# Optimization experiments

Measured on AMD Instinct MI355X. Metric: run time of the kernel, lower is better.

Reference implementation:

```python
import jax, jax.numpy as jnp
import numpy as np


def setup_inputs() -> dict:
    key = jax.random.key(0)
    ks = jax.random.split(key, 8)
    B, L, D = 4, 2048, 2048
    H, Dh, S = 24, 64, 64
    Di = H * Dh              # 1536
    P = H * (1 + 2 * S)      # 3096
    return {
        "hidden_states": jax.random.normal(ks[0], (B, L, D), jnp.float32),
        "norm_w": jnp.ones((D,), jnp.float32),
        "in_proj_w": jax.random.normal(ks[1], (2 * Di, D), jnp.float32) * 0.02,
        "in_proj_b": jnp.zeros((2 * Di,), jnp.float32),
        "conv_w": jax.random.normal(ks[2], (Di, 1, 4), jnp.float32) * 0.2,
        "conv_b": jnp.zeros((Di,), jnp.float32),
        "x_proj_w": jax.random.normal(ks[3], (P, Di), jnp.float32) * 0.02,
        "x_proj_b": jnp.zeros((P,), jnp.float32),
        "A_log": jnp.full((H,), np.log(0.5), jnp.float32),
        "log2_alpha_base": jnp.full((H,), -1.0, jnp.float32),
        "log2_beta": jnp.zeros((H,), jnp.float32),
        "surprise_ema": jnp.ones((H,), jnp.float32),
        "out_proj_w": jax.random.normal(ks[4], (D, Di), jnp.float32) * 0.02,
        "out_proj_b": jnp.zeros((D,), jnp.float32),
        "res_gate": jnp.full((1,), 1.0 / np.sqrt(2 * 24), jnp.float32),
    }


def reference(hidden_states, norm_w, in_proj_w, in_proj_b, conv_w, conv_b,
              x_proj_w, x_proj_b, A_log, log2_alpha_base, log2_beta,
              surprise_ema, out_proj_w, out_proj_b, res_gate):
    Bsz, L, D = hidden_states.shape
    H = A_log.shape[0]
    S = (x_proj_b.shape[0] // H - 1) // 2
    Di = in_proj_w.shape[0] // 2
    Dh = Di // H
    eps = jnp.finfo(jnp.float32).eps

    # RMSNorm
    x = hidden_states * jax.lax.rsqrt(jnp.mean(hidden_states ** 2, -1, keepdims=True) + eps) * norm_w
    # in_proj -> split x/z
    xz = x @ in_proj_w.T + in_proj_b
    x, z = xz[..., :Di], xz[..., Di:]
    # causal depthwise conv1d (kernel 4, left pad 3 == torch pad=3 then [:, :L])
    xc = jax.lax.conv_general_dilated(
        x.transpose(0, 2, 1), conv_w, (1,), [(3, 0)],
        dimension_numbers=("NCH", "OIH", "NCH"), feature_group_count=Di)
    x = jax.nn.silu((xc + conv_b[None, :, None]).transpose(0, 2, 1))
    # x_proj -> dt, B, C
    xp = (x @ x_proj_w.T + x_proj_b).reshape(Bsz, L, H, 1 + 2 * S)
    dt = xp[..., 0]
    Bs = xp[..., 1:1 + S]
    Cs = xp[..., 1 + S:]
    Bs = Bs / jnp.maximum(jnp.linalg.norm(Bs, axis=-1, keepdims=True), 1e-12)
    Cs = Cs / jnp.maximum(jnp.linalg.norm(Cs, axis=-1, keepdims=True), 1e-12)
    # dt-scaled log decay (dt_scale = softplus(dt))
    A = jnp.clip(A_log, -2.3, -0.01)[None, None, :] * jax.nn.softplus(dt)
    A_decay = jnp.exp(A)                       # [B, L, H]
    X = x.reshape(Bsz, L, H, Dh)

    # surprise-gate constants (eval mode: EMA buffer fixed)
    alpha_base = 1.0 - 2.0 ** jnp.clip(log2_alpha_base, -3.32, -0.015)   # [H]
    beta = 2.0 ** jnp.clip(log2_beta, -2.0, 2.0)                          # [H]

    def step(carry, xs):
        h, h_red = carry                      # [B,H,S,Dh], [B,H,S]
        x_t, a_t, B_t, C_t = xs               # [B,H,Dh], [B,H], [B,H,S], [B,H,S]
        u_red = B_t * x_t.mean(-1)[..., None]                 # mean over Dh of outer product
        diff = (1.0 - a_t)[..., None] * u_red                 # h_new_reduced - h_expected
        pe = jnp.mean(diff ** 2, -1)                          # [B,H]
        ns = pe / (surprise_ema[None, :] + 1e-6)
        boost = jax.nn.relu(jnp.tanh(beta[None, :] * ns))
        alpha = jnp.clip(alpha_base[None, :] + (1.0 - alpha_base[None, :]) * boost, 0.01, 0.999)
        u_t = B_t[..., None] * x_t[:, :, None, :]             # [B,H,S,Dh]
        h = alpha[..., None, None] * h + (1.0 - alpha)[..., None, None] * u_t
        h_red = h.mean(-1)
        y = jnp.einsum("bhs,bhsd->bhd", C_t, h)
        return (h, h_red), y

    h0 = jnp.zeros((Bsz, H, S, Dh), jnp.float32)
    hr0 = jnp.zeros((Bsz, H, S), jnp.float32)
    xs = (X.transpose(1, 0, 2, 3), A_decay.transpose(1, 0, 2),
          Bs.transpose(1, 0, 2, 3), Cs.transpose(1, 0, 2, 3))
    _, Yt = jax.lax.scan(step, (h0, hr0), xs)                 # [L,B,H,Dh]
    Y = Yt.transpose(1, 0, 2, 3).reshape(Bsz, L, Di)
    Y = Y * jax.nn.silu(z)
    out = Y @ out_proj_w.T + out_proj_b
    return hidden_states + res_gate * out
```

## Files before the change

kernel.cpp:

```cpp
#include <hip/hip_runtime.h>
#include <stdint.h>

#define BB 4
#define LLEN 2048
#define DMODEL 2048
#define NH 24
#define DH 64
#define SS 64
#define DI 1536
#define N2 3072
#define NP 3096
#define NP_PAD 3200
#define MROWS 8192
#define NCHUNK 16
#define QC 128
#define XP2LD 136
#define WBLK 56064

using bf16x8 = __bf16 __attribute__((ext_vector_type(8)));
using f32x4  = float __attribute__((ext_vector_type(4)));

__device__ __forceinline__ unsigned short f2bf(float f) {
  union { float f; unsigned int u; } v; v.f = f;
  unsigned int u = v.u + 0x7fffu + ((v.u >> 16) & 1u);
  return (unsigned short)(u >> 16);
}
__device__ __forceinline__ float bf2f(unsigned short h) {
  union { unsigned int u; float f; } v; v.u = ((unsigned int)h) << 16;
  return v.f;
}

__device__ __forceinline__ void gload16(const void* g, void* l) {
  __builtin_amdgcn_global_load_lds(
    reinterpret_cast<const __attribute__((address_space(1))) void*>(reinterpret_cast<uintptr_t>(g)),
    reinterpret_cast<__attribute__((address_space(3))) void*>((uint32_t)(reinterpret_cast<uintptr_t>(l))),
    16, 0, 0);
}

__global__ __launch_bounds__(256) void k_pre(
    const float* __restrict__ in_w, unsigned short* __restrict__ wA,
    const float* __restrict__ xw, unsigned short* __restrict__ wX,
    const float* __restrict__ ow, unsigned short* __restrict__ wO,
    const float* __restrict__ hs, const float* __restrict__ norm_w,
    unsigned short* __restrict__ xnorm,
    const float* __restrict__ A_log, const float* __restrict__ l2ab,
    const float* __restrict__ l2b, const float* __restrict__ se,
    float* __restrict__ hc) {
  const int blk = blockIdx.x;
  const int t = threadIdx.x;
  if (blk < WBLK) {
    int i = blk * 256 + t;
    if (i < N2 * DMODEL) { wA[i] = f2bf(in_w[i]); return; }
    i -= N2 * DMODEL;
    if (i < NP_PAD * DI) { wX[i] = (i < NP * DI) ? f2bf(xw[i]) : (unsigned short)0; return; }
    i -= NP_PAD * DI;
    wO[i] = f2bf(ow[i]);
    return;
  }
  if (blk == WBLK + MROWS) {
    if (t < NH) {
      hc[t]          = fminf(fmaxf(A_log[t], -2.3f), -0.01f);
      hc[NH + t]     = exp2f(fminf(fmaxf(l2b[t], -2.f), 2.f));
      hc[2 * NH + t] = 1.f - exp2f(fminf(fmaxf(l2ab[t], -3.32f), -0.015f));
      hc[3 * NH + t] = 1.f / (se[t] + 1e-6f);
    }
    return;
  }
  const int row = blk - WBLK;
  const float* x = hs + (size_t)row * DMODEL;
  float4 v0 = reinterpret_cast<const float4*>(x)[t * 2 + 0];
  float4 v1 = reinterpret_cast<const float4*>(x)[t * 2 + 1];
  float ss = v0.x * v0.x + v0.y * v0.y + v0.z * v0.z + v0.w * v0.w +
             v1.x * v1.x + v1.y * v1.y + v1.z * v1.z + v1.w * v1.w;
#pragma unroll
  for (int o = 32; o; o >>= 1) ss += __shfl_xor(ss, o);
  __shared__ float red[4];
  if ((t & 63) == 0) red[t >> 6] = ss;
  __syncthreads();
  ss = red[0] + red[1] + red[2] + red[3];
  const float r = rsqrtf(ss * (1.0f / DMODEL) + 1.1920928955078125e-07f);
  float4 w0 = reinterpret_cast<const float4*>(norm_w)[t * 2 + 0];
  float4 w1 = reinterpret_cast<const float4*>(norm_w)[t * 2 + 1];
  union { unsigned short u[8]; uint4 v; } pk;
  pk.u[0] = f2bf(v0.x * r * w0.x); pk.u[1] = f2bf(v0.y * r * w0.y);
  pk.u[2] = f2bf(v0.z * r * w0.z); pk.u[3] = f2bf(v0.w * r * w0.w);
  pk.u[4] = f2bf(v1.x * r * w1.x); pk.u[5] = f2bf(v1.y * r * w1.y);
  pk.u[6] = f2bf(v1.z * r * w1.z); pk.u[7] = f2bf(v1.w * r * w1.w);
  *reinterpret_cast<uint4*>(xnorm + (size_t)row * DMODEL + t * 8) = pk.v;
}

template <int EPI>
__global__ __launch_bounds__(512, 2)
void k_gemm6(const unsigned short* __restrict__ A, const unsigned short* __restrict__ B,
             const float* __restrict__ bias, void* __restrict__ Cv,
             const float* __restrict__ resid, const float* __restrict__ gatep,
             float* __restrict__ dtbuf,
             int K, int NT_N, int Nout, int ldc) {
  constexpr int AELEM = 128 * 64;
  constexpr int BUFE = AELEM + 16384;
  __shared__ alignas(16) unsigned short sm[3 * BUFE];
  const int tid = threadIdx.x;
  const int lane = tid & 63, wid = tid >> 6;
  const int wm = wid >> 2, wn = wid & 3;
  const int fr = lane & 15, kg = lane >> 4;
  const int nwg = gridDim.x;
  const int wg = ((int)blockIdx.x & 7) * (nwg >> 3) + ((int)blockIdx.x >> 3);
  const int m0 = (wg / NT_N) * 128, n0 = (wg % NT_N) * 256;
  const int NT = K >> 6;

  const unsigned short* asrc[2];
  const unsigned short* bsrc[4];
#pragma unroll
  for (int li = 0; li < 2; ++li) {
    const int gi = li * 512 + tid, r = gi >> 3, q = gi & 7;
    asrc[li] = A + (size_t)(m0 + r) * K + ((q ^ (r & 7)) << 3);
  }
#pragma unroll
  for (int li = 0; li < 4; ++li) {
    const int gi = li * 512 + tid, r = gi >> 3, q = gi & 7;
    bsrc[li] = B + (size_t)(n0 + r) * K + ((q ^ (r & 7)) << 3);
  }
  const int wlds = wid * 64;

#define STG6(buf, ko)                                                          \
  { unsigned short* da_ = sm + (buf) * BUFE;                                   \
    gload16(asrc[0] + (ko), da_ + ((0 * 512 + wlds) << 3));                    \
    gload16(asrc[1] + (ko), da_ + ((1 * 512 + wlds) << 3));                    \
    unsigned short* db_ = sm + (buf) * BUFE + AELEM;                           \
    _Pragma("unroll") for (int li = 0; li < 4; ++li)                           \
      gload16(bsrc[li] + (ko), db_ + ((li * 512 + wlds) << 3)); }

#define ARD6(bufp, f, kk)                                                      \
  (*(const bf16x8*)((bufp) + (wm * 64 + (f) * 16 + fr) * 64 +                  \
      ((((kk) * 4 + kg) ^ (fr & 7)) << 3)))
#define BRD6(bufp, nf, kk)                                                     \
  (*(const bf16x8*)((bufp) + AELEM + (wn * 64 + (nf) * 16 + fr) * 64 +         \
      ((((kk) * 4 + kg) ^ (fr & 7)) << 3)))

  f32x4 acc[4][4] = {};

  STG6(0, 0)
  STG6(1, 64)
  asm volatile("s_waitcnt vmcnt(6)" ::: "memory");
  __builtin_amdgcn_s_barrier();

  int bc_i = 0;
  for (int t = 0; t < NT; ++t) {
    unsigned short* bc = sm + bc_i * BUFE;
    const int bn_i = (bc_i + 2 >= 3) ? (bc_i - 1) : (bc_i + 2);
    const bool st = (t + 2) < NT;
    if (st) STG6(bn_i, (t + 2) << 6)

    bf16x8 bfv[4][2], af[4][2];
#pragma unroll
    for (int nf = 0; nf < 4; ++nf) {
      bfv[nf][0] = BRD6(bc, nf, 0);
      bfv[nf][1] = BRD6(bc, nf, 1);
    }
#pragma unroll
    for (int mf = 0; mf < 4; ++mf) {
      af[mf][0] = ARD6(bc, mf, 0);
      af[mf][1] = ARD6(bc, mf, 1);
    }
    __builtin_amdgcn_sched_barrier(0);
    asm volatile("s_waitcnt lgkmcnt(0)" ::: "memory");
    __builtin_amdgcn_sched_barrier(0);
    __builtin_amdgcn_s_setprio(1);
#pragma unroll
    for (int mf = 0; mf < 4; ++mf)
#pragma unroll
      for (int nf = 0; nf < 4; ++nf)
#pragma unroll
        for (int kk = 0; kk < 2; ++kk)
          acc[mf][nf] = __builtin_amdgcn_mfma_f32_16x16x32_bf16(
              af[mf][kk], bfv[nf][kk], acc[mf][nf], 0, 0, 0);
    __builtin_amdgcn_s_setprio(0);

    if (st) { asm volatile("s_waitcnt vmcnt(6)" ::: "memory"); }
    else    { asm volatile("s_waitcnt vmcnt(0)" ::: "memory"); }
    __builtin_amdgcn_s_barrier();
    bc_i = (bc_i + 1 >= 3) ? 0 : (bc_i + 1);
  }

  float* Cf = (float*)Cv;
  unsigned short* Ch = (unsigned short*)Cv;
  const float rg = (EPI == 2) ? gatep[0] : 0.f;
#pragma unroll
  for (int nf = 0; nf < 4; ++nf) {
    const int col = n0 + wn * 64 + nf * 16 + fr;
    if (col >= Nout) continue;
    const float bv = bias[col];
    if (EPI == 3) {
      const int h = col / 129;
      const int e = col - h * 129;
      if (e == 0) {
#pragma unroll
        for (int mf = 0; mf < 4; ++mf) {
          const int rowb = m0 + wm * 64 + mf * 16 + kg * 4;
#pragma unroll
          for (int r = 0; r < 4; ++r) {
            const int row = rowb + r;
            const size_t r2 = (((size_t)((row >> 11) * NH + h)) << 11) + (row & (LLEN - 1));
            dtbuf[r2] = acc[mf][nf][r] + bv;
          }
        }
      } else {
        const int ep = e - 1;
#pragma unroll
        for (int mf = 0; mf < 4; ++mf) {
          const int rowb = m0 + wm * 64 + mf * 16 + kg * 4;
#pragma unroll
          for (int r = 0; r < 4; ++r) {
            const int row = rowb + r;
            const size_t dst =
                (((size_t)((row >> 11) * NH + h) << 11) + (row & (LLEN - 1))) * XP2LD + ep;
            Ch[dst] = f2bf(acc[mf][nf][r] + bv);
          }
        }
      }
    } else {
#pragma unroll
      for (int mf = 0; mf < 4; ++mf) {
        const int rowb = m0 + wm * 64 + mf * 16 + kg * 4;
#pragma unroll
        for (int r = 0; r < 4; ++r) {
          const size_t o = (size_t)(rowb + r) * ldc + col;
          float v = acc[mf][nf][r] + bv;
          if (EPI == 1) {
            Ch[o] = f2bf(v);
          } else {
            v = resid[o] + rg * v;
            Cf[o] = v;
          }
        }
      }
    }
  }
#undef STG6
#undef ARD6
#undef BRD6
}

__global__ __launch_bounds__(256) void k_alpha(const float* __restrict__ dtbuf,
                                               const float* __restrict__ xmean,
                                               const float* __restrict__ hc,
                                               float* __restrict__ al) {
  const int i = blockIdx.x * 256 + threadIdx.x;
  const int h = (i >> 11) % NH;
  const float dt = dtbuf[i];
  const float sp = (dt > 20.f) ? dt : log1pf(expf(dt));
  const float one_a = 1.f - expf(hc[h] * sp);
  const float xm = xmean[i];
  const float pe = one_a * one_a * xm * xm * (1.f / 64.f);
  const float boost = fmaxf(tanhf(hc[NH + h] * pe * hc[3 * NH + h]), 0.f);
  const float ab = hc[2 * NH + h];
  al[i] = fminf(fmaxf(ab + (1.f - ab) * boost, 0.01f), 0.999f);
}

__global__ __launch_bounds__(256) void k_dwconv(const unsigned short* __restrict__ xz,
                                                const float* __restrict__ cw,
                                                const float* __restrict__ cb,
                                                unsigned short* __restrict__ out,
                                                float* __restrict__ xmean) {
  const int idx = blockIdx.x * 256 + threadIdx.x;
  const int c0 = (idx % 192) * 8;
  const int bl0 = (idx / 192) * 4;
  const int lpos0 = bl0 & (LLEN - 1);
  float w[8][4];
#pragma unroll
  for (int j = 0; j < 8; ++j) {
    const float4 wv = *(const float4*)(cw + (c0 + j) * 4);
    w[j][0] = wv.x; w[j][1] = wv.y; w[j][2] = wv.z; w[j][3] = wv.w;
  }
  float xr[7][8];
#pragma unroll
  for (int m = 0; m < 7; ++m) {
    uint4 xv = make_uint4(0u, 0u, 0u, 0u);
    if (lpos0 - 3 + m >= 0)
      xv = *(const uint4*)(xz + (size_t)(bl0 - 3 + m) * N2 + c0);
    const unsigned short* xs = (const unsigned short*)&xv;
#pragma unroll
    for (int j = 0; j < 8; ++j) xr[m][j] = bf2f(xs[j]);
  }
  const float4 cb0 = *(const float4*)(cb + c0);
  const float4 cb1 = *(const float4*)(cb + c0 + 4);
  const float cbv[8] = {cb0.x, cb0.y, cb0.z, cb0.w, cb1.x, cb1.y, cb1.z, cb1.w};
  float hsum[4] = {0.f, 0.f, 0.f, 0.f};
#pragma unroll
  for (int t4 = 0; t4 < 4; ++t4) {
    union { unsigned short u[8]; uint4 v; } pk;
#pragma unroll
    for (int j = 0; j < 8; ++j) {
      float a = cbv[j];
#pragma unroll
      for (int k = 0; k < 4; ++k) a = fmaf(w[j][k], xr[t4 + k][j], a);
      a = a / (1.f + __expf(-a));
      hsum[t4] += a;
      pk.u[j] = f2bf(a);
    }
    *(uint4*)(out + (size_t)(bl0 + t4) * DI + c0) = pk.v;
  }
#pragma unroll
  for (int o = 1; o < 8; o <<= 1) {
#pragma unroll
    for (int t4 = 0; t4 < 4; ++t4) hsum[t4] += __shfl_xor(hsum[t4], o);
  }
  if ((threadIdx.x & 7) == 0) {
    const int h = (idx % 192) >> 3;
    const int b = bl0 >> 11;
    float4 xm = make_float4(hsum[0] * (1.f / 64.f), hsum[1] * (1.f / 64.f),
                            hsum[2] * (1.f / 64.f), hsum[3] * (1.f / 64.f));
    *(float4*)(xmean + (((size_t)(b * NH + h)) << 11) + lpos0) = xm;
  }
}

__global__ __launch_bounds__(256) void k_chunk1(
    const unsigned short* __restrict__ xp2, const unsigned short* __restrict__ xcg,
    const float* __restrict__ al, unsigned short* __restrict__ xz,
    unsigned short* __restrict__ Hbuf, float* __restrict__ Dc) {
  const int blk = blockIdx.x;
  const int bh = blk >> 4, c = blk & 15;
  const int b = bh / NH, h = bh % NH;
  const int tid = threadIdx.x, w = tid >> 6, lane = tid & 63;
  const int fr = lane & 15, kg = lane >> 4;
  const int rbase = b * LLEN + c * QC;
  const size_t rbase2 = ((size_t)bh << 11) + c * QC;

  __shared__ float lc[QC], ia[QC], escl[QC], rbA[QC], rcC[QC];
  __shared__ float wtot[2];
  __shared__ alignas(16) unsigned short XT[64][152];
  __shared__ alignas(16) unsigned short BsT[64][152];
  __shared__ alignas(16) unsigned short Pt[128][88];

  float a = 1.f, la = 0.f;
  if (tid < QC) { a = al[(size_t)bh * LLEN + c * QC + tid]; la = __logf(a); }
  float s = la;
#pragma unroll
  for (int o = 1; o < 64; o <<= 1) { float t2 = __shfl_up(s, o); if (lane >= o) s += t2; }
  if (tid < QC && lane == 63) wtot[w] = s;
  __syncthreads();
  if (tid < QC) { lc[tid] = s + ((w == 1) ? wtot[0] : 0.f); ia[tid] = 1.f - a; }
  __syncthreads();
  const float lcE = lc[QC - 1];
  if (tid < QC) escl[tid] = __expf(lcE - lc[tid]);
  if (tid == 0) Dc[blk] = __expf(lcE);
  __syncthreads();

  {
    const int r8 = tid >> 3, q8 = tid & 7;
#pragma unroll
    for (int it = 0; it < 4; ++it) {
      const int u = it * 32 + r8;
      const uint4 xv = *(const uint4*)(xcg + (size_t)(rbase + u) * DI + h * DH + q8 * 8);
      const unsigned short* xs = (const unsigned short*)&xv;
#pragma unroll
      for (int j = 0; j < 8; ++j) XT[q8 * 8 + j][u] = xs[j];
      const size_t prow = (rbase2 + u) * XP2LD;
      const uint4 bv = *(const uint4*)(xp2 + prow + q8 * 8);
      const uint4 cv = *(const uint4*)(xp2 + prow + 64 + q8 * 8);
      const unsigned short* bsv = (const unsigned short*)&bv;
      const unsigned short* csv = (const unsigned short*)&cv;
      float bb[8], sb = 0.f, sc2 = 0.f;
#pragma unroll
      for (int j = 0; j < 8; ++j) {
        bb[j] = bf2f(bsv[j]);
        sb = fmaf(bb[j], bb[j], sb);
        const float cc = bf2f(csv[j]);
        sc2 = fmaf(cc, cc, sc2);
      }
      sb += __shfl_xor(sb, 1); sb += __shfl_xor(sb, 2); sb += __shfl_xor(sb, 4);
      sc2 += __shfl_xor(sc2, 1); sc2 += __shfl_xor(sc2, 2); sc2 += __shfl_xor(sc2, 4);
      const float rcpB = 1.f / fmaxf(sqrtf(sb), 1e-12f);
      const float e = escl[u] * ia[u] * rcpB;
#pragma unroll
      for (int j = 0; j < 8; ++j) BsT[q8 * 8 + j][u] = f2bf(bb[j] * e);
      if (q8 == 0) {
        rbA[u] = ia[u] * rcpB;
        rcC[u] = 1.f / fmaxf(sqrtf(sc2), 1e-12f);
      }
    }
  }
  __syncthreads();

  bf16x8 cf[2][2];
#pragma unroll
  for (int fi = 0; fi < 2; ++fi)
#pragma unroll
    for (int kk = 0; kk < 2; ++kk) {
      const int t = w * 32 + fi * 16 + fr;
      const uint4 v = *(const uint4*)(xp2 + (rbase2 + t) * XP2LD + 64 + kk * 32 + kg * 8);
      cf[fi][kk] = *(const bf16x8*)&v;
    }

  float lct[2][4], rct[2][4];
#pragma unroll
  for (int fi = 0; fi < 2; ++fi)
#pragma unroll
    for (int r = 0; r < 4; ++r) {
      const int t = w * 32 + fi * 16 + kg * 4 + r;
      lct[fi][r] = lc[t];
      rct[fi][r] = rcC[t];
    }

  f32x4 yacc[2][4] = {};
  f32x4 hacc[4] = {};
#pragma unroll
  for (int ut = 0; ut < 2; ++ut) {
    f32x4 g[2][4] = {};
#pragma unroll
    for (int kk = 0; kk < 2; ++kk)
#pragma unroll
      for (int fj = 0; fj < 4; ++fj) {
        const int u = ut * 64 + fj * 16 + fr;
        const uint4 v = *(const uint4*)(xp2 + (rbase2 + u) * XP2LD + kk * 32 + kg * 8);
        const bf16x8 bfrag = *(const bf16x8*)&v;
#pragma unroll
        for (int fi = 0; fi < 2; ++fi)
          g[fi][fj] = __builtin_amdgcn_mfma_f32_16x16x32_bf16(cf[fi][kk], bfrag, g[fi][fj], 0, 0, 0);
      }
#pragma unroll
    for (int fi = 0; fi < 2; ++fi)
#pragma unroll
      for (int fj = 0; fj < 4; ++fj) {
        const int u = ut * 64 + fj * 16 + fr;
        const float lcu = lc[u], sbu = rbA[u];
#pragma unroll
        for (int r = 0; r < 4; ++r) {
          const int t = w * 32 + fi * 16 + kg * 4 + r;
          const float v = (t >= u) ? g[fi][fj][r] * __expf(lct[fi][r] - lcu) * sbu * rct[fi][r] : 0.f;
          Pt[t][fj * 16 + fr] = f2bf(v);
        }
      }
#pragma unroll
    for (int kk = 0; kk < 2; ++kk) {
      bf16x8 xf[4];
#pragma unroll
      for (int fj = 0; fj < 4; ++fj)
        xf[fj] = *(const bf16x8*)&XT[fj * 16 + fr][ut * 64 + kk * 32 + kg * 8];
      bf16x8 pf[2];
#pragma unroll
      for (int fi = 0; fi < 2; ++fi)
        pf[fi] = *(const bf16x8*)&Pt[w * 32 + fi * 16 + fr][kk * 32 + kg * 8];
#pragma unroll
      for (int fi = 0; fi < 2; ++fi)
#pragma unroll
        for (int fj = 0; fj < 4; ++fj)
          yacc[fi][fj] = __builtin_amdgcn_mfma_f32_16x16x32_bf16(pf[fi], xf[fj], yacc[fi][fj], 0, 0, 0);
      const bf16x8 xh = *(const bf16x8*)&XT[w * 16 + fr][ut * 64 + kk * 32 + kg * 8];
#pragma unroll
      for (int fi = 0; fi < 4; ++fi) {
        const bf16x8 bs = *(const bf16x8*)&BsT[fi * 16 + fr][ut * 64 + kk * 32 + kg * 8];
        hacc[fi] = __builtin_amdgcn_mfma_f32_16x16x32_bf16(bs, xh, hacc[fi], 0, 0, 0);
      }
    }
  }
#pragma unroll
  for (int fi = 0; fi < 2; ++fi)
#pragma unroll
    for (int fj = 0; fj < 4; ++fj)
#pragma unroll
      for (int r = 0; r < 4; ++r) {
        const int t = w * 32 + fi * 16 + kg * 4 + r;
        const int d = fj * 16 + fr;
        xz[(size_t)(rbase + t) * N2 + h * DH + d] = f2bf(yacc[fi][fj][r]);
      }
  const int dcol = w * 16 + fr;
#pragma unroll
  for (int fi = 0; fi < 4; ++fi) {
    ushort4 pk;
    pk.x = f2bf(hacc[fi][0]); pk.y = f2bf(hacc[fi][1]);
    pk.z = f2bf(hacc[fi][2]); pk.w = f2bf(hacc[fi][3]);
    *(ushort4*)(Hbuf + ((size_t)blk * 64 + dcol) * 64 + fi * 16 + kg * 4) = pk;
  }
}

__global__ __launch_bounds__(256) void k_carry(unsigned short* __restrict__ Hbuf,
                                               const float* __restrict__ Dc) {
  const int bh = blockIdx.x, tid = threadIdx.x;
  float carry[16];
#pragma unroll
  for (int j = 0; j < 16; ++j) carry[j] = 0.f;
  for (int c = 0; c < NCHUNK; ++c) {
    unsigned short* p = Hbuf + (((size_t)(bh * NCHUNK + c)) << 12) + tid * 16;
    const uint4 v0 = *(const uint4*)(p);
    const uint4 v1 = *(const uint4*)(p + 8);
    const unsigned short* hs0 = (const unsigned short*)&v0;
    const unsigned short* hs1 = (const unsigned short*)&v1;
    float hl[16];
#pragma unroll
    for (int j = 0; j < 8; ++j) { hl[j] = bf2f(hs0[j]); hl[8 + j] = bf2f(hs1[j]); }
    uint4 o0, o1;
    unsigned short* os0 = (unsigned short*)&o0;
    unsigned short* os1 = (unsigned short*)&o1;
#pragma unroll
    for (int j = 0; j < 8; ++j) { os0[j] = f2bf(carry[j]); os1[j] = f2bf(carry[8 + j]); }
    *(uint4*)(p) = o0;
    *(uint4*)(p + 8) = o1;
    const float dc = Dc[bh * NCHUNK + c];
#pragma unroll
    for (int j = 0; j < 16; ++j) carry[j] = fmaf(dc, carry[j], hl[j]);
  }
}

__global__ __launch_bounds__(256) void k_chunk2(
    const unsigned short* __restrict__ xp2, const float* __restrict__ al,
    const unsigned short* __restrict__ Hbuf, const unsigned short* __restrict__ xz,
    unsigned short* __restrict__ xcg) {
  const int blk = blockIdx.x;
  const int bh = blk >> 4, c = blk & 15;
  const int b = bh / NH, h = bh % NH;
  const int tid = threadIdx.x, w = tid >> 6, lane = tid & 63;
  const int fr = lane & 15, kg = lane >> 4;
  const int rbase = b * LLEN + c * QC;
  const size_t rbase2 = ((size_t)bh << 11) + c * QC;
  __shared__ float lc[QC], rc2[QC];
  __shared__ float wtot[2];
  float a = 1.f, la = 0.f;
  if (tid < QC) { a = al[(size_t)bh * LLEN + c * QC + tid]; la = __logf(a); }
  float s = la;
#pragma unroll
  for (int o = 1; o < 64; o <<= 1) { float t2 = __shfl_up(s, o); if (lane >= o) s += t2; }
  if (tid < QC && lane == 63) wtot[w] = s;
  __syncthreads();
  if (tid < QC) lc[tid] = s + ((w == 1) ? wtot[0] : 0.f);
  __syncthreads();
  bf16x8 cf[2][2];
#pragma unroll
  for (int fi = 0; fi < 2; ++fi) {
    const int t = w * 32 + fi * 16 + fr;
    float ss = 0.f;
#pragma unroll
    for (int kk = 0; kk < 2; ++kk) {
      const uint4 v = *(const uint4*)(xp2 + (rbase2 + t) * XP2LD + 64 + kk * 32 + kg * 8);
      cf[fi][kk] = *(const bf16x8*)&v;
      const unsigned short* cs = (const unsigned short*)&v;
#pragma unroll
      for (int q = 0; q < 8; ++q) { const float cc = bf2f(cs[q]); ss = fmaf(cc, cc, ss); }
    }
    ss += __shfl_xor(ss, 16);
    ss += __shfl_xor(ss, 32);
    if (kg == 0) rc2[t] = 1.f / fmaxf(sqrtf(ss), 1e-12f);
  }
  bf16x8 hf[4][2];
#pragma unroll
  for (int fj = 0; fj < 4; ++fj)
#pragma unroll
    for (int kk = 0; kk < 2; ++kk) {
      const uint4 v = *(const uint4*)(Hbuf + ((size_t)blk * 64 + fj * 16 + fr) * 64 + kk * 32 + kg * 8);
      hf[fj][kk] = *(const bf16x8*)&v;
    }
  __syncthreads();
  f32x4 y[2][4] = {};
#pragma unroll
  for (int kk = 0; kk < 2; ++kk)
#pragma unroll
    for (int fi = 0; fi < 2; ++fi)
#pragma unroll
      for (int fj = 0; fj < 4; ++fj)
        y[fi][fj] = __builtin_amdgcn_mfma_f32_16x16x32_bf16(cf[fi][kk], hf[fj][kk], y[fi][fj], 0, 0, 0);
#pragma unroll
  for (int fi = 0; fi < 2; ++fi)
#pragma unroll
    for (int fj = 0; fj < 4; ++fj)
#pragma unroll
      for (int r = 0; r < 4; ++r) {
        const int t = w * 32 + fi * 16 + kg * 4 + r;
        const int d = fj * 16 + fr;
        const float scl = rc2[t] * __expf(lc[t]);
        const size_t rowg = (size_t)(rbase + t);
        const float yv = y[fi][fj][r] * scl + bf2f(xz[rowg * N2 + h * DH + d]);
        const float zv = bf2f(xz[rowg * N2 + DI + h * DH + d]);
        const float g = yv * (zv / (1.f + __expf(-zv)));
        xcg[rowg * DI + h * DH + d] = f2bf(g);
      }
}

extern "C" void kernel_launch(void* const* d_in, const int* in_sizes, int n_in,
                              void* d_out, int out_size, void* d_ws, size_t ws_size,
                              hipStream_t stream) {
  const float* hs     = (const float*)d_in[0];
  const float* norm_w = (const float*)d_in[1];
  const float* in_w   = (const float*)d_in[2];
  const float* in_b   = (const float*)d_in[3];
  const float* cw     = (const float*)d_in[4];
  const float* cb     = (const float*)d_in[5];
  const float* xw     = (const float*)d_in[6];
  const float* xb     = (const float*)d_in[7];
  const float* A_log  = (const float*)d_in[8];
  const float* l2ab   = (const float*)d_in[9];
  const float* l2b    = (const float*)d_in[10];
  const float* se     = (const float*)d_in[11];
  const float* ow     = (const float*)d_in[12];
  const float* ob     = (const float*)d_in[13];
  const float* rg     = (const float*)d_in[14];
  float* out = (float*)d_out;

  char* ws = (char*)d_ws;
  unsigned short* xnorm = (unsigned short*)(ws);
  unsigned short* wA    = (unsigned short*)(ws + 33554432ull);
  unsigned short* wX    = (unsigned short*)(ws + 46137344ull);
  unsigned short* wO    = (unsigned short*)(ws + 55967744ull);
  unsigned short* xz    = (unsigned short*)(ws + 62259200ull);
  unsigned short* xp2   = (unsigned short*)(ws + 112590848ull);
  float* xmean          = (float*)(ws + 166068224ull);
  float* al             = (float*)(ws + 166854656ull);
  float* Dc             = (float*)(ws + 167641088ull);
  float* hc             = (float*)(ws + 167647232ull);
  float* dtbuf          = (float*)(ws + 167651328ull);
  unsigned short* xcg   = xnorm;
  unsigned short* Hbuf  = wA;

  k_pre<<<WBLK + MROWS + 1, 256, 0, stream>>>(in_w, wA, xw, wX, ow, wO,
                                              hs, norm_w, xnorm,
                                              A_log, l2ab, l2b, se, hc);
  k_gemm6<1><<<768, 512, 0, stream>>>(xnorm, wA, in_b, xz, nullptr, nullptr,
                                      nullptr, DMODEL, 12, N2, N2);
  k_dwconv<<<(MROWS / 4) * 192 / 256, 256, 0, stream>>>(xz, cw, cb, xcg, xmean);
  k_gemm6<3><<<832, 512, 0, stream>>>(xcg, wX, xb, xp2, nullptr, nullptr,
                                      dtbuf, DI, 13, NP, 0);
  k_alpha<<<(BB * NH * LLEN) / 256, 256, 0, stream>>>(dtbuf, xmean, hc, al);
  k_chunk1<<<BB * NH * NCHUNK, 256, 0, stream>>>(xp2, xcg, al, xz, Hbuf, Dc);
  k_carry<<<BB * NH, 256, 0, stream>>>(Hbuf, Dc);
  k_chunk2<<<BB * NH * NCHUNK, 256, 0, stream>>>(xp2, al, Hbuf, xz, xcg);
  k_gemm6<2><<<512, 512, 0, stream>>>(xcg, wO, ob, out, hs, rg,
                                      nullptr, DI, 8, DMODEL, DMODEL);
}
```

Baseline: 442.8 us.

## Retile GEMMs to 128x192 with double buffering and higher occupancy target

The bf16 MFMA GEMM kernel's N tile shrinks from 256 to 192 columns, and the triple-buffered LDS pipeline becomes double-buffered with a full vmcnt(0) wait each iteration. Launch bounds now target 4 waves per SIMD instead of 2, and grid sizes are recomputed for all three GEMMs. The aim is to fit more workgroups per CU, through less LDS and fewer accumulator registers, and to improve tile balance across CUs. The cost is less prefetch depth, so memory latency is hidden only by occupancy. The out_proj and x_proj tiles now read weight rows past the padded weight buffers; those columns are masked in the epilogue.

```diff
diff --git a/kernel.cpp b/kernel.cpp
--- a/kernel.cpp
+++ b/kernel.cpp
@@ -90,77 +90,75 @@
 }
 
 template <int EPI>
-__global__ __launch_bounds__(512, 2)
-void k_gemm6(const unsigned short* __restrict__ A, const unsigned short* __restrict__ B,
+__global__ __launch_bounds__(512, 4)
+void k_gemm7(const unsigned short* __restrict__ A, const unsigned short* __restrict__ B,
              const float* __restrict__ bias, void* __restrict__ Cv,
              const float* __restrict__ resid, const float* __restrict__ gatep,
              float* __restrict__ dtbuf,
              int K, int NT_N, int Nout, int ldc) {
   constexpr int AELEM = 128 * 64;
-  constexpr int BUFE = AELEM + 16384;
-  __shared__ alignas(16) unsigned short sm[3 * BUFE];
+  constexpr int BELEM = 192 * 64;
+  constexpr int BUFE = AELEM + BELEM;
+  __shared__ alignas(16) unsigned short sm[2 * BUFE];
   const int tid = threadIdx.x;
   const int lane = tid & 63, wid = tid >> 6;
   const int wm = wid >> 2, wn = wid & 3;
   const int fr = lane & 15, kg = lane >> 4;
   const int nwg = gridDim.x;
   const int wg = ((int)blockIdx.x & 7) * (nwg >> 3) + ((int)blockIdx.x >> 3);
-  const int m0 = (wg / NT_N) * 128, n0 = (wg % NT_N) * 256;
+  const int m0 = (wg / NT_N) * 128, n0 = (wg % NT_N) * 192;
   const int NT = K >> 6;
 
   const unsigned short* asrc[2];
-  const unsigned short* bsrc[4];
+  const unsigned short* bsrc[3];
 #pragma unroll
   for (int li = 0; li < 2; ++li) {
     const int gi = li * 512 + tid, r = gi >> 3, q = gi & 7;
     asrc[li] = A + (size_t)(m0 + r) * K + ((q ^ (r & 7)) << 3);
   }
 #pragma unroll
-  for (int li = 0; li < 4; ++li) {
+  for (int li = 0; li < 3; ++li) {
     const int gi = li * 512 + tid, r = gi >> 3, q = gi & 7;
     bsrc[li] = B + (size_t)(n0 + r) * K + ((q ^ (r & 7)) << 3);
   }
   const int wlds = wid * 64;
 
-#define STG6(buf, ko)                                                          \
+#define STG7(buf, ko)                                                          \
   { unsigned short* da_ = sm + (buf) * BUFE;                                   \
     gload16(asrc[0] + (ko), da_ + ((0 * 512 + wlds) << 3));                    \
     gload16(asrc[1] + (ko), da_ + ((1 * 512 + wlds) << 3));                    \
     unsigned short* db_ = sm + (buf) * BUFE + AELEM;                           \
-    _Pragma("unroll") for (int li = 0; li < 4; ++li)                           \
-      gload16(bsrc[li] + (ko), db_ + ((li * 512 + wlds) << 3)); }
-
-#define ARD6(bufp, f, kk)                                                      \
+    gload16(bsrc[0] + (ko), db_ + ((0 * 512 + wlds) << 3));                    \
+    gload16(bsrc[1] + (ko), db_ + ((1 * 512 + wlds) << 3));                    \
+    gload16(bsrc[2] + (ko), db_ + ((2 * 512 + wlds) << 3)); }
+
+#define ARD7(bufp, f, kk)                                                      \
   (*(const bf16x8*)((bufp) + (wm * 64 + (f) * 16 + fr) * 64 +                  \
       ((((kk) * 4 + kg) ^ (fr & 7)) << 3)))
-#define BRD6(bufp, nf, kk)                                                     \
-  (*(const bf16x8*)((bufp) + AELEM + (wn * 64 + (nf) * 16 + fr) * 64 +         \
+#define BRD7(bufp, nf, kk)                                                     \
+  (*(const bf16x8*)((bufp) + AELEM + (wn * 48 + (nf) * 16 + fr) * 64 +         \
       ((((kk) * 4 + kg) ^ (fr & 7)) << 3)))
 
-  f32x4 acc[4][4] = {};
-
-  STG6(0, 0)
-  STG6(1, 64)
-  asm volatile("s_waitcnt vmcnt(6)" ::: "memory");
+  f32x4 acc[4][3] = {};
+
+  STG7(0, 0)
+  asm volatile("s_waitcnt vmcnt(0)" ::: "memory");
   __builtin_amdgcn_s_barrier();
 
-  int bc_i = 0;
   for (int t = 0; t < NT; ++t) {
-    unsigned short* bc = sm + bc_i * BUFE;
-    const int bn_i = (bc_i + 2 >= 3) ? (bc_i - 1) : (bc_i + 2);
-    const bool st = (t + 2) < NT;
-    if (st) STG6(bn_i, (t + 2) << 6)
-
-    bf16x8 bfv[4][2], af[4][2];
-#pragma unroll
-    for (int nf = 0; nf < 4; ++nf) {
-      bfv[nf][0] = BRD6(bc, nf, 0);
-      bfv[nf][1] = BRD6(bc, nf, 1);
+    unsigned short* bc = sm + (t & 1) * BUFE;
+    if (t + 1 < NT) STG7((t & 1) ^ 1, (t + 1) << 6)
+
+    bf16x8 bfv[3][2], af[4][2];
+#pragma unroll
+    for (int nf = 0; nf < 3; ++nf) {
+      bfv[nf][0] = BRD7(bc, nf, 0);
+      bfv[nf][1] = BRD7(bc, nf, 1);
     }
 #pragma unroll
     for (int mf = 0; mf < 4; ++mf) {
-      af[mf][0] = ARD6(bc, mf, 0);
-      af[mf][1] = ARD6(bc, mf, 1);
+      af[mf][0] = ARD7(bc, mf, 0);
+      af[mf][1] = ARD7(bc, mf, 1);
     }
     __builtin_amdgcn_sched_barrier(0);
     asm volatile("s_waitcnt lgkmcnt(0)" ::: "memory");
@@ -169,25 +167,23 @@
 #pragma unroll
     for (int mf = 0; mf < 4; ++mf)
 #pragma unroll
-      for (int nf = 0; nf < 4; ++nf)
+      for (int nf = 0; nf < 3; ++nf)
 #pragma unroll
         for (int kk = 0; kk < 2; ++kk)
           acc[mf][nf] = __builtin_amdgcn_mfma_f32_16x16x32_bf16(
               af[mf][kk], bfv[nf][kk], acc[mf][nf], 0, 0, 0);
     __builtin_amdgcn_s_setprio(0);
 
-    if (st) { asm volatile("s_waitcnt vmcnt(6)" ::: "memory"); }
-    else    { asm volatile("s_waitcnt vmcnt(0)" ::: "memory"); }
+    asm volatile("s_waitcnt vmcnt(0)" ::: "memory");
     __builtin_amdgcn_s_barrier();
-    bc_i = (bc_i + 1 >= 3) ? 0 : (bc_i + 1);
   }
 
   float* Cf = (float*)Cv;
   unsigned short* Ch = (unsigned short*)Cv;
   const float rg = (EPI == 2) ? gatep[0] : 0.f;
 #pragma unroll
-  for (int nf = 0; nf < 4; ++nf) {
-    const int col = n0 + wn * 64 + nf * 16 + fr;
+  for (int nf = 0; nf < 3; ++nf) {
+    const int col = n0 + wn * 48 + nf * 16 + fr;
     if (col >= Nout) continue;
     const float bv = bias[col];
     if (EPI == 3) {
@@ -236,9 +232,9 @@
       }
     }
   }
-#undef STG6
-#undef ARD6
-#undef BRD6
+#undef STG7
+#undef ARD7
+#undef BRD7
 }
 
 __global__ __launch_bounds__(256) void k_alpha(const float* __restrict__ dtbuf,
@@ -613,15 +609,15 @@
   k_pre<<<WBLK + MROWS + 1, 256, 0, stream>>>(in_w, wA, xw, wX, ow, wO,
                                               hs, norm_w, xnorm,
                                               A_log, l2ab, l2b, se, hc);
-  k_gemm6<1><<<768, 512, 0, stream>>>(xnorm, wA, in_b, xz, nullptr, nullptr,
-                                      nullptr, DMODEL, 12, N2, N2);
+  k_gemm7<1><<<1024, 512, 0, stream>>>(xnorm, wA, in_b, xz, nullptr, nullptr,
+                                       nullptr, DMODEL, 16, N2, N2);
   k_dwconv<<<(MROWS / 4) * 192 / 256, 256, 0, stream>>>(xz, cw, cb, xcg, xmean);
-  k_gemm6<3><<<832, 512, 0, stream>>>(xcg, wX, xb, xp2, nullptr, nullptr,
-                                      dtbuf, DI, 13, NP, 0);
+  k_gemm7<3><<<1088, 512, 0, stream>>>(xcg, wX, xb, xp2, nullptr, nullptr,
+                                       dtbuf, DI, 17, NP, 0);
   k_alpha<<<(BB * NH * LLEN) / 256, 256, 0, stream>>>(dtbuf, xmean, hc, al);
   k_chunk1<<<BB * NH * NCHUNK, 256, 0, stream>>>(xp2, xcg, al, xz, Hbuf, Dc);
   k_carry<<<BB * NH, 256, 0, stream>>>(Hbuf, Dc);
   k_chunk2<<<BB * NH * NCHUNK, 256, 0, stream>>>(xp2, al, Hbuf, xz, xcg);
-  k_gemm6<2><<<512, 512, 0, stream>>>(xcg, wO, ob, out, hs, rg,
-                                      nullptr, DI, 8, DMODEL, DMODEL);
-}
+  k_gemm7<2><<<704, 512, 0, stream>>>(xcg, wO, ob, out, hs, rg,
+                                      nullptr, DI, 11, DMODEL, DMODEL);
+}
```

Result: faster. 417.8 us (-5.6%).
